# Performance work log

Measured on AMD Instinct MI355X. Metric: run time of the kernel, lower is better.

The kernel has to match this reference:

```python
import jax, jax.numpy as jnp
import numpy as np

EPS_STAB = 1e-9   # numerical_stabilizer default
BN_EPS = 1e-5     # flax BatchNorm default epsilon


def setup_inputs() -> dict:
    key = jax.random.key(0)
    ks = jax.random.split(key, 5)
    B, N, C = 2, 4096, 512
    s = 1.0 / np.sqrt(C)
    d = {"inputs": jax.random.normal(ks[0], (B, N, C), jnp.float32)}
    # 1x1 convs == pointwise linear maps [C_in, C_out] + bias
    for i, w in enumerate(["Wq", "Wk", "Wv", "Wo"]):
        d[w] = jax.random.normal(ks[1 + i], (C, C), jnp.float32) * s
    for b in ["bq", "bk", "bv", "bo"]:
        d[b] = jnp.zeros((C,), jnp.float32)
    # BatchNorm (inference: use_running_average=True since train=False)
    d["bn_scale"] = jnp.ones((C,), jnp.float32)
    d["bn_bias"] = jnp.zeros((C,), jnp.float32)
    d["bn_mean"] = jnp.zeros((C,), jnp.float32)
    d["bn_var"] = jnp.ones((C,), jnp.float32)
    return d


def reference(inputs, Wq, bq, Wk, bk, Wv, bv, Wo, bo,
              bn_scale, bn_bias, bn_mean, bn_var):
    # QKV via 1x1 conv == dense projection. [B, N, C]
    q = inputs @ Wq + bq
    k = inputs @ Wk + bk
    v = inputs @ Wv + bv
    # scores [B, M, N]; softmax over last axis (N)
    att = jax.nn.softmax(jnp.einsum('bmc,bnc->bmn', q, k), axis=-1)
    # non-standard renorm: divide by column sums (axis=1 == M axis)
    att = att / (EPS_STAB + jnp.sum(att, axis=1, keepdims=True))
    # faithful to einsum '...MN,...NC->...NC': sum attention over M, scale v
    out = v * jnp.sum(att, axis=1)[..., None]
    # output 1x1 conv
    out = out @ Wo + bo
    # BatchNorm with running stats (feature axis -1)
    out = (out - bn_mean) * jax.lax.rsqrt(bn_var + BN_EPS) * bn_scale + bn_bias
    return jax.nn.relu(out) + inputs
```

## Files before the change

kernel.cpp:

```cpp
#include <hip/hip_runtime.h>
#include <hip/hip_bf16.h>

typedef unsigned short u16;
typedef __attribute__((ext_vector_type(8))) short short8;
typedef __attribute__((ext_vector_type(4))) float f32x4;

__device__ __forceinline__ u16 f2bf(float f) {
    union { float f; unsigned u; } v; v.f = f;
    unsigned r = v.u + 0x7fffu + ((v.u >> 16) & 1u);
    return (u16)(r >> 16);
}

__device__ __forceinline__ float fexp2(float x) {
#if __has_builtin(__builtin_amdgcn_exp2f)
    return __builtin_amdgcn_exp2f(x);
#else
    return __expf(x * 0.6931471805599453f);
#endif
}

__device__ __forceinline__ void async_cp16(const u16* g, u16* l) {
    __builtin_amdgcn_global_load_lds(
        (const __attribute__((address_space(1))) void*)g,
        (__attribute__((address_space(3))) void*)l, 16, 0, 0);
}

__device__ __forceinline__ void gemm512(const u16* __restrict__ A,
                                        const u16* __restrict__ B,
                                        u16* As, u16* Bs,
                                        f32x4 acc[4][4], int tid) {
    const int lane = tid & 63, w = tid >> 6;
    const int quad = lane >> 4, l15 = lane & 15;
    const int wm = tid >> 7, wn = (tid >> 6) & 1;
    const int srow0 = w * 32 + (lane >> 2);
    const int srow1 = srow0 + 16;
    const int scol = (lane & 3) * 8;
    u16* la0 = As + (w * 2 + 0) * 512;
    u16* la1 = As + (w * 2 + 1) * 512;
    u16* lb0 = Bs + (w * 2 + 0) * 512;
    u16* lb1 = Bs + (w * 2 + 1) * 512;
    for (int k0 = 0; k0 < 512; k0 += 32) {
        __syncthreads();
        async_cp16(A + (size_t)srow0 * 512 + k0 + scol, la0);
        async_cp16(A + (size_t)srow1 * 512 + k0 + scol, la1);
        async_cp16(B + (size_t)srow0 * 512 + k0 + scol, lb0);
        async_cp16(B + (size_t)srow1 * 512 + k0 + scol, lb1);
        __syncthreads();
        short8 af[4], bfr[4];
#pragma unroll
        for (int i = 0; i < 4; i++)
            af[i] = *(const short8*)&As[(wm * 64 + i * 16 + l15) * 32 + quad * 8];
#pragma unroll
        for (int j = 0; j < 4; j++)
            bfr[j] = *(const short8*)&Bs[(wn * 64 + j * 16 + l15) * 32 + quad * 8];
#pragma unroll
        for (int i = 0; i < 4; i++)
#pragma unroll
            for (int j = 0; j < 4; j++)
                acc[i][j] = __builtin_amdgcn_mfma_f32_16x16x32_bf16(
                    af[i], bfr[j], acc[i][j], 0, 0, 0);
    }
}

__global__ void convert_x(const float* __restrict__ X, u16* __restrict__ Xb) {
    int idx = (blockIdx.x * 256 + threadIdx.x) * 4;
    float4 v = *(const float4*)&X[idx];
    ushort4 o;
    o.x = f2bf(v.x); o.y = f2bf(v.y); o.z = f2bf(v.z); o.w = f2bf(v.w);
    *(ushort4*)&Xb[idx] = o;
}

__global__ void transpose_w(const float* __restrict__ W0, const float* __restrict__ W1,
                            const float* __restrict__ W2, const float* __restrict__ W3,
                            u16* __restrict__ T0, u16* __restrict__ T1,
                            u16* __restrict__ T2, u16* __restrict__ T3) {
    const float* src; u16* dst;
    switch (blockIdx.z) {
        case 0: src = W0; dst = T0; break;
        case 1: src = W1; dst = T1; break;
        case 2: src = W2; dst = T2; break;
        default: src = W3; dst = T3; break;
    }
    __shared__ float tile[32][33];
    int bo_ = blockIdx.x * 32;
    int bi  = blockIdx.y * 32;
#pragma unroll
    for (int t = 0; t < 4; t++) {
        int i = bi + threadIdx.y + t * 8;
        tile[threadIdx.y + t * 8][threadIdx.x] = src[i * 512 + bo_ + threadIdx.x];
    }
    __syncthreads();
#pragma unroll
    for (int t = 0; t < 4; t++) {
        int o = bo_ + threadIdx.y + t * 8;
        dst[o * 512 + bi + threadIdx.x] = f2bf(tile[threadIdx.x][threadIdx.y + t * 8]);
    }
}

__global__ __launch_bounds__(256) void gemm_qkv(
    const u16* __restrict__ Xb, const u16* __restrict__ Wall,
    const float* __restrict__ bq, const float* __restrict__ bk,
    const float* __restrict__ bv, u16* __restrict__ Qall) {
    __shared__ __align__(16) u16 As[128 * 32];
    __shared__ __align__(16) u16 Bs[128 * 32];
    int tid = threadIdx.x;
    int m0 = blockIdx.x * 128, n0 = blockIdx.y * 128, z = blockIdx.z;
    const u16* Bt = Wall + (size_t)z * 262144 + (size_t)n0 * 512;
    const float* bias = (z == 0) ? bq : (z == 1) ? bk : bv;
    const float qs = (z == 0) ? 1.44269504088896340736f : 1.0f;
    u16* C = Qall + (size_t)z * 4194304;
    f32x4 acc[4][4];
#pragma unroll
    for (int i = 0; i < 4; i++)
#pragma unroll
        for (int j = 0; j < 4; j++) acc[i][j] = (f32x4){0.f, 0.f, 0.f, 0.f};
    gemm512(Xb + (size_t)m0 * 512, Bt, As, Bs, acc, tid);
    int lane = tid & 63, quad = lane >> 4, l15 = lane & 15;
    int wm = tid >> 7, wn = (tid >> 6) & 1;
#pragma unroll
    for (int j = 0; j < 4; j++) {
        int n = n0 + wn * 64 + j * 16 + l15;
        float bvv = bias[n];
#pragma unroll
        for (int i = 0; i < 4; i++)
#pragma unroll
            for (int rg = 0; rg < 4; rg++) {
                int m = m0 + wm * 64 + i * 16 + quad * 4 + rg;
                C[(size_t)m * 512 + n] = f2bf((acc[i][j][rg] + bvv) * qs);
            }
    }
}

__global__ __launch_bounds__(256) void attn_pass1(
    const u16* __restrict__ Qb, const u16* __restrict__ Kb,
    float2* __restrict__ statsP) {
    __shared__ __align__(16) u16 As[128 * 32];
    __shared__ __align__(16) u16 Bs[128 * 32];
    int tid = threadIdx.x;
    int mblk = blockIdx.x, nch = blockIdx.y, b = blockIdx.z;
    const u16* Q = Qb + ((size_t)(b * 4096 + mblk * 128)) * 512;
    int lane = tid & 63, quad = lane >> 4, l15 = lane & 15;
    int wm = tid >> 7, wn = (tid >> 6) & 1;
    float runM[4][4], runL[4][4];
#pragma unroll
    for (int i = 0; i < 4; i++)
#pragma unroll
        for (int rg = 0; rg < 4; rg++) { runM[i][rg] = -INFINITY; runL[i][rg] = 0.f; }
    for (int nt = 0; nt < 4; nt++) {
        const u16* K = Kb + ((size_t)(b * 4096 + nch * 512 + nt * 128)) * 512;
        f32x4 acc[4][4];
#pragma unroll
        for (int i = 0; i < 4; i++)
#pragma unroll
            for (int j = 0; j < 4; j++) acc[i][j] = (f32x4){0.f, 0.f, 0.f, 0.f};
        gemm512(Q, K, As, Bs, acc, tid);
#pragma unroll
        for (int i = 0; i < 4; i++)
#pragma unroll
            for (int rg = 0; rg < 4; rg++) {
                float v0 = acc[i][0][rg], v1 = acc[i][1][rg];
                float v2 = acc[i][2][rg], v3 = acc[i][3][rg];
                float vm = fmaxf(fmaxf(v0, v1), fmaxf(v2, v3));
                float mo = runM[i][rg];
                if (vm > mo - 30.f) {
                    float nm = fmaxf(mo, vm);
                    runL[i][rg] = runL[i][rg] * fexp2(mo - nm) +
                                  fexp2(v0 - nm) + fexp2(v1 - nm) +
                                  fexp2(v2 - nm) + fexp2(v3 - nm);
                    runM[i][rg] = nm;
                }
            }
    }
#pragma unroll
    for (int i = 0; i < 4; i++)
#pragma unroll
        for (int rg = 0; rg < 4; rg++) {
            float M = runM[i][rg], L = runL[i][rg];
#pragma unroll
            for (int d = 1; d < 16; d <<= 1) {
                float Mo = __shfl_xor(M, d);
                float Lo = __shfl_xor(L, d);
                float Mn = fmaxf(M, Mo);
                L = L * fexp2(M - Mn) + Lo * fexp2(Mo - Mn);
                M = Mn;
            }
            if (l15 == 0)
                statsP[((size_t)(b * 16 + nch * 2 + wn)) * 4096 +
                       mblk * 128 + wm * 64 + i * 16 + quad * 4 + rg] =
                    make_float2(M, L);
        }
}

__global__ void reduce_stats(const float2* __restrict__ statsP,
                             float* __restrict__ cstat) {
    int t = blockIdx.x * 256 + threadIdx.x;
    int b = t >> 12, m = t & 4095;
    float2 p[16];
    float M = -INFINITY;
#pragma unroll
    for (int ch = 0; ch < 16; ch++) {
        p[ch] = statsP[((size_t)(b * 16 + ch)) * 4096 + m];
        M = fmaxf(M, p[ch].x);
    }
    float L = 0.f;
#pragma unroll
    for (int ch = 0; ch < 16; ch++) L += p[ch].y * fexp2(p[ch].x - M);
    cstat[t] = M + __log2f(L);
}

__global__ __launch_bounds__(256) void attn_pass2(
    const u16* __restrict__ Qb, const u16* __restrict__ Kb,
    const float* __restrict__ cstat, float* __restrict__ Sg) {
    __shared__ __align__(16) u16 As[128 * 32];
    __shared__ __align__(16) u16 Bs[128 * 32];
    int tid = threadIdx.x;
    int nblk = blockIdx.x, mch = blockIdx.y, b = blockIdx.z;
    const u16* K = Kb + ((size_t)(b * 4096 + nblk * 128)) * 512;
    int lane = tid & 63, quad = lane >> 4, l15 = lane & 15;
    int wm = tid >> 7, wn = (tid >> 6) & 1;
    float cp0 = 0.f, cp1 = 0.f, cp2 = 0.f, cp3 = 0.f;
    for (int mt = 0; mt < 4; mt++) {
        int m0 = mch * 512 + mt * 128;
        const u16* Q = Qb + ((size_t)(b * 4096 + m0)) * 512;
        f32x4 acc[4][4];
#pragma unroll
        for (int i = 0; i < 4; i++)
#pragma unroll
            for (int j = 0; j < 4; j++) acc[i][j] = (f32x4){0.f, 0.f, 0.f, 0.f};
        gemm512(Q, K, As, Bs, acc, tid);
        float4 c4[4];
#pragma unroll
        for (int i = 0; i < 4; i++)
            c4[i] = *(const float4*)&cstat[b * 4096 + m0 + wm * 64 + i * 16 + quad * 4];
#pragma unroll
        for (int i = 0; i < 4; i++) {
            float cc[4] = {c4[i].x, c4[i].y, c4[i].z, c4[i].w};
#pragma unroll
            for (int rg = 0; rg < 4; rg++) {
                float c = cc[rg];
                float v0 = acc[i][0][rg] - c, v1 = acc[i][1][rg] - c;
                float v2 = acc[i][2][rg] - c, v3 = acc[i][3][rg] - c;
                float vm = fmaxf(fmaxf(v0, v1), fmaxf(v2, v3));
                if (vm > -60.f) {
                    cp0 += fexp2(v0); cp1 += fexp2(v1);
                    cp2 += fexp2(v2); cp3 += fexp2(v3);
                }
            }
        }
    }
    float cps[4] = {cp0, cp1, cp2, cp3};
#pragma unroll
    for (int j = 0; j < 4; j++) {
        float s = cps[j];
        s += __shfl_xor(s, 16);
        s += __shfl_xor(s, 32);
        if (lane < 16)
            atomicAdd(&Sg[b * 4096 + nblk * 128 + wn * 64 + j * 16 + lane], s);
    }
}

__global__ __launch_bounds__(256) void gemm_final(
    const u16* __restrict__ A, const u16* __restrict__ Bt,
    const float* __restrict__ Sg, const float* __restrict__ bo,
    const float* __restrict__ g, const float* __restrict__ bb,
    const float* __restrict__ mean, const float* __restrict__ var,
    const float* __restrict__ X, float* __restrict__ out) {
    __shared__ __align__(16) u16 As[128 * 32];
    __shared__ __align__(16) u16 Bs[128 * 32];
    int tid = threadIdx.x;
    int m0 = blockIdx.x * 128, n0 = blockIdx.y * 128;
    f32x4 acc[4][4];
#pragma unroll
    for (int i = 0; i < 4; i++)
#pragma unroll
        for (int j = 0; j < 4; j++) acc[i][j] = (f32x4){0.f, 0.f, 0.f, 0.f};
    gemm512(A + (size_t)m0 * 512, Bt + (size_t)n0 * 512, As, Bs, acc, tid);
    int lane = tid & 63, quad = lane >> 4, l15 = lane & 15;
    int wm = tid >> 7, wn = (tid >> 6) & 1;
    float sc[4][4];
#pragma unroll
    for (int i = 0; i < 4; i++) {
        float4 s = *(const float4*)&Sg[m0 + wm * 64 + i * 16 + quad * 4];
        float v[4] = {s.x, s.y, s.z, s.w};
#pragma unroll
        for (int rg = 0; rg < 4; rg++) sc[i][rg] = v[rg] / (1e-9f + v[rg]);
    }
#pragma unroll
    for (int j = 0; j < 4; j++) {
        int n = n0 + wn * 64 + j * 16 + l15;
        float aj = rsqrtf(var[n] + 1e-5f) * g[n];
        float cj = bb[n] - mean[n] * aj;
        float bj = bo[n];
#pragma unroll
        for (int i = 0; i < 4; i++)
#pragma unroll
            for (int rg = 0; rg < 4; rg++) {
                int m = m0 + wm * 64 + i * 16 + quad * 4 + rg;
                float x = acc[i][j][rg] * sc[i][rg] + bj;
                float y = x * aj + cj;
                out[(size_t)m * 512 + n] = fmaxf(y, 0.f) + X[(size_t)m * 512 + n];
            }
    }
}

extern "C" void kernel_launch(void* const* d_in, const int* in_sizes, int n_in,
                              void* d_out, int out_size, void* d_ws, size_t ws_size,
                              hipStream_t stream) {
    const float* X  = (const float*)d_in[0];
    const float* Wq = (const float*)d_in[1];
    const float* Wk = (const float*)d_in[2];
    const float* Wv = (const float*)d_in[3];
    const float* Wo = (const float*)d_in[4];
    const float* bq = (const float*)d_in[5];
    const float* bk = (const float*)d_in[6];
    const float* bv = (const float*)d_in[7];
    const float* bo = (const float*)d_in[8];
    const float* g    = (const float*)d_in[9];
    const float* bb   = (const float*)d_in[10];
    const float* mean = (const float*)d_in[11];
    const float* var  = (const float*)d_in[12];
    float* out = (float*)d_out;

    char* ws = (char*)d_ws;
    u16* Xb  = (u16*)(ws + 0);
    u16* Wqt = (u16*)(ws + 8388608);
    u16* Wkt = (u16*)(ws + 8912896);
    u16* Wvt = (u16*)(ws + 9437184);
    u16* Wot = (u16*)(ws + 9961472);
    u16* Qb  = (u16*)(ws + 10485760);
    u16* Kb  = (u16*)(ws + 18874368);
    u16* Vb  = (u16*)(ws + 27262976);
    float2* statsP = (float2*)(ws + 35651584);
    float* cstat   = (float*)(ws + 36700160);
    float* Sg      = (float*)(ws + 36765696);

    convert_x<<<4096, 256, 0, stream>>>(X, Xb);
    transpose_w<<<dim3(16, 16, 4), dim3(32, 8), 0, stream>>>(
        Wq, Wk, Wv, Wo, Wqt, Wkt, Wvt, Wot);
    gemm_qkv<<<dim3(64, 4, 3), 256, 0, stream>>>(Xb, Wqt, bq, bk, bv, Qb);
    attn_pass1<<<dim3(32, 8, 2), 256, 0, stream>>>(Qb, Kb, statsP);
    reduce_stats<<<32, 256, 0, stream>>>(statsP, cstat);
    hipMemsetAsync(Sg, 0, 2 * 4096 * sizeof(float), stream);
    attn_pass2<<<dim3(32, 8, 2), 256, 0, stream>>>(Qb, Kb, cstat, Sg);
    gemm_final<<<dim3(64, 4), 256, 0, stream>>>(Vb, Wot, Sg, bo, g, bb, mean, var,
                                                X, out);
}
```

Before: 235.0 us.

## Double attention grid split, merge prep kernels, fold memset, shrink final GEMM tile

The two attention passes now split the key/query range into 16 chunks of 256 instead of 8 of 512, doubling the grid from 512 to 1024 blocks to fill more compute units. The stats partials grow to 32 per row. The pass-1 shuffle merge is simplified to a max-reduce followed by a sum-reduce. The X conversion and weight transpose are merged into one prep launch, and the Sg zeroing moves into reduce_stats, removing a launch and a memset. The final GEMM uses 64-row tiles to double its block count. The cost is more partial-stat traffic and more redundant Q/K tile loads per block.

```diff
diff --git a/kernel.cpp b/kernel.cpp
--- a/kernel.cpp
+++ b/kernel.cpp
@@ -62,38 +62,78 @@
     }
 }
 
-__global__ void convert_x(const float* __restrict__ X, u16* __restrict__ Xb) {
-    int idx = (blockIdx.x * 256 + threadIdx.x) * 4;
-    float4 v = *(const float4*)&X[idx];
-    ushort4 o;
-    o.x = f2bf(v.x); o.y = f2bf(v.y); o.z = f2bf(v.z); o.w = f2bf(v.w);
-    *(ushort4*)&Xb[idx] = o;
-}
-
-__global__ void transpose_w(const float* __restrict__ W0, const float* __restrict__ W1,
-                            const float* __restrict__ W2, const float* __restrict__ W3,
-                            u16* __restrict__ T0, u16* __restrict__ T1,
-                            u16* __restrict__ T2, u16* __restrict__ T3) {
+__device__ __forceinline__ void gemm512_r64(const u16* __restrict__ A,
+                                            const u16* __restrict__ B,
+                                            u16* As, u16* Bs,
+                                            f32x4 acc[2][4], int tid) {
+    const int lane = tid & 63, w = tid >> 6;
+    const int quad = lane >> 4, l15 = lane & 15;
+    const int wm = tid >> 7, wn = (tid >> 6) & 1;
+    const int srowA = w * 16 + (lane >> 2);
+    const int srowB0 = (w * 2 + 0) * 16 + (lane >> 2);
+    const int srowB1 = (w * 2 + 1) * 16 + (lane >> 2);
+    const int scol = (lane & 3) * 8;
+    u16* la = As + w * 512;
+    u16* lb0 = Bs + (w * 2 + 0) * 512;
+    u16* lb1 = Bs + (w * 2 + 1) * 512;
+    for (int k0 = 0; k0 < 512; k0 += 32) {
+        __syncthreads();
+        async_cp16(A + (size_t)srowA * 512 + k0 + scol, la);
+        async_cp16(B + (size_t)srowB0 * 512 + k0 + scol, lb0);
+        async_cp16(B + (size_t)srowB1 * 512 + k0 + scol, lb1);
+        __syncthreads();
+        short8 af[2], bfr[4];
+#pragma unroll
+        for (int i = 0; i < 2; i++)
+            af[i] = *(const short8*)&As[(wm * 32 + i * 16 + l15) * 32 + quad * 8];
+#pragma unroll
+        for (int j = 0; j < 4; j++)
+            bfr[j] = *(const short8*)&Bs[(wn * 64 + j * 16 + l15) * 32 + quad * 8];
+#pragma unroll
+        for (int i = 0; i < 2; i++)
+#pragma unroll
+            for (int j = 0; j < 4; j++)
+                acc[i][j] = __builtin_amdgcn_mfma_f32_16x16x32_bf16(
+                    af[i], bfr[j], acc[i][j], 0, 0, 0);
+    }
+}
+
+__global__ void prep(const float* __restrict__ X, const float* __restrict__ W0,
+                     const float* __restrict__ W1, const float* __restrict__ W2,
+                     const float* __restrict__ W3, u16* __restrict__ Xb,
+                     u16* __restrict__ T0, u16* __restrict__ T1,
+                     u16* __restrict__ T2, u16* __restrict__ T3) {
+    __shared__ float tile[32][33];
+    int id = blockIdx.x, tid = threadIdx.x;
+    if (id < 4096) {
+        int idx = (id * 256 + tid) * 4;
+        float4 v = *(const float4*)&X[idx];
+        ushort4 o;
+        o.x = f2bf(v.x); o.y = f2bf(v.y); o.z = f2bf(v.z); o.w = f2bf(v.w);
+        *(ushort4*)&Xb[idx] = o;
+        return;
+    }
+    int t = id - 4096;
+    int z = t >> 8, rem = t & 255;
+    int bo_ = (rem & 15) * 32, bi = (rem >> 4) * 32;
     const float* src; u16* dst;
-    switch (blockIdx.z) {
+    switch (z) {
         case 0: src = W0; dst = T0; break;
         case 1: src = W1; dst = T1; break;
         case 2: src = W2; dst = T2; break;
         default: src = W3; dst = T3; break;
     }
-    __shared__ float tile[32][33];
-    int bo_ = blockIdx.x * 32;
-    int bi  = blockIdx.y * 32;
-#pragma unroll
-    for (int t = 0; t < 4; t++) {
-        int i = bi + threadIdx.y + t * 8;
-        tile[threadIdx.y + t * 8][threadIdx.x] = src[i * 512 + bo_ + threadIdx.x];
+    int tx = tid & 31, ty = tid >> 5;
+#pragma unroll
+    for (int s = 0; s < 4; s++) {
+        int i = bi + ty + s * 8;
+        tile[ty + s * 8][tx] = src[i * 512 + bo_ + tx];
     }
     __syncthreads();
 #pragma unroll
-    for (int t = 0; t < 4; t++) {
-        int o = bo_ + threadIdx.y + t * 8;
-        dst[o * 512 + bi + threadIdx.x] = f2bf(tile[threadIdx.x][threadIdx.y + t * 8]);
+    for (int s = 0; s < 4; s++) {
+        int o = bo_ + ty + s * 8;
+        dst[o * 512 + bi + tx] = f2bf(tile[tx][ty + s * 8]);
     }
 }
 
@@ -146,8 +186,8 @@
     for (int i = 0; i < 4; i++)
 #pragma unroll
         for (int rg = 0; rg < 4; rg++) { runM[i][rg] = -INFINITY; runL[i][rg] = 0.f; }
-    for (int nt = 0; nt < 4; nt++) {
-        const u16* K = Kb + ((size_t)(b * 4096 + nch * 512 + nt * 128)) * 512;
+    for (int nt = 0; nt < 2; nt++) {
+        const u16* K = Kb + ((size_t)(b * 4096 + nch * 256 + nt * 128)) * 512;
         f32x4 acc[4][4];
 #pragma unroll
         for (int i = 0; i < 4; i++)
@@ -175,37 +215,36 @@
     for (int i = 0; i < 4; i++)
 #pragma unroll
         for (int rg = 0; rg < 4; rg++) {
-            float M = runM[i][rg], L = runL[i][rg];
-#pragma unroll
-            for (int d = 1; d < 16; d <<= 1) {
-                float Mo = __shfl_xor(M, d);
-                float Lo = __shfl_xor(L, d);
-                float Mn = fmaxf(M, Mo);
-                L = L * fexp2(M - Mn) + Lo * fexp2(Mo - Mn);
-                M = Mn;
-            }
+            float M = runM[i][rg];
+            float Mf = M;
+#pragma unroll
+            for (int d = 1; d < 16; d <<= 1) Mf = fmaxf(Mf, __shfl_xor(Mf, d));
+            float L = runL[i][rg] * fexp2(M - Mf);
+#pragma unroll
+            for (int d = 1; d < 16; d <<= 1) L += __shfl_xor(L, d);
             if (l15 == 0)
-                statsP[((size_t)(b * 16 + nch * 2 + wn)) * 4096 +
+                statsP[((size_t)(b * 32 + nch * 2 + wn)) * 4096 +
                        mblk * 128 + wm * 64 + i * 16 + quad * 4 + rg] =
-                    make_float2(M, L);
+                    make_float2(Mf, L);
         }
 }
 
 __global__ void reduce_stats(const float2* __restrict__ statsP,
-                             float* __restrict__ cstat) {
+                             float* __restrict__ cstat, float* __restrict__ Sg) {
     int t = blockIdx.x * 256 + threadIdx.x;
     int b = t >> 12, m = t & 4095;
-    float2 p[16];
     float M = -INFINITY;
-#pragma unroll
-    for (int ch = 0; ch < 16; ch++) {
-        p[ch] = statsP[((size_t)(b * 16 + ch)) * 4096 + m];
+    float2 p[32];
+#pragma unroll
+    for (int ch = 0; ch < 32; ch++) {
+        p[ch] = statsP[((size_t)(b * 32 + ch)) * 4096 + m];
         M = fmaxf(M, p[ch].x);
     }
     float L = 0.f;
 #pragma unroll
-    for (int ch = 0; ch < 16; ch++) L += p[ch].y * fexp2(p[ch].x - M);
+    for (int ch = 0; ch < 32; ch++) L += p[ch].y * fexp2(p[ch].x - M);
     cstat[t] = M + __log2f(L);
+    Sg[t] = 0.f;
 }
 
 __global__ __launch_bounds__(256) void attn_pass2(
@@ -219,8 +258,8 @@
     int lane = tid & 63, quad = lane >> 4, l15 = lane & 15;
     int wm = tid >> 7, wn = (tid >> 6) & 1;
     float cp0 = 0.f, cp1 = 0.f, cp2 = 0.f, cp3 = 0.f;
-    for (int mt = 0; mt < 4; mt++) {
-        int m0 = mch * 512 + mt * 128;
+    for (int mt = 0; mt < 2; mt++) {
+        int m0 = mch * 256 + mt * 128;
         const u16* Q = Qb + ((size_t)(b * 4096 + m0)) * 512;
         f32x4 acc[4][4];
 #pragma unroll
@@ -265,22 +304,22 @@
     const float* __restrict__ g, const float* __restrict__ bb,
     const float* __restrict__ mean, const float* __restrict__ var,
     const float* __restrict__ X, float* __restrict__ out) {
-    __shared__ __align__(16) u16 As[128 * 32];
+    __shared__ __align__(16) u16 As[64 * 32];
     __shared__ __align__(16) u16 Bs[128 * 32];
     int tid = threadIdx.x;
-    int m0 = blockIdx.x * 128, n0 = blockIdx.y * 128;
-    f32x4 acc[4][4];
-#pragma unroll
-    for (int i = 0; i < 4; i++)
+    int m0 = blockIdx.x * 64, n0 = blockIdx.y * 128;
+    f32x4 acc[2][4];
+#pragma unroll
+    for (int i = 0; i < 2; i++)
 #pragma unroll
         for (int j = 0; j < 4; j++) acc[i][j] = (f32x4){0.f, 0.f, 0.f, 0.f};
-    gemm512(A + (size_t)m0 * 512, Bt + (size_t)n0 * 512, As, Bs, acc, tid);
+    gemm512_r64(A + (size_t)m0 * 512, Bt + (size_t)n0 * 512, As, Bs, acc, tid);
     int lane = tid & 63, quad = lane >> 4, l15 = lane & 15;
     int wm = tid >> 7, wn = (tid >> 6) & 1;
-    float sc[4][4];
-#pragma unroll
-    for (int i = 0; i < 4; i++) {
-        float4 s = *(const float4*)&Sg[m0 + wm * 64 + i * 16 + quad * 4];
+    float sc[2][4];
+#pragma unroll
+    for (int i = 0; i < 2; i++) {
+        float4 s = *(const float4*)&Sg[m0 + wm * 32 + i * 16 + quad * 4];
         float v[4] = {s.x, s.y, s.z, s.w};
 #pragma unroll
         for (int rg = 0; rg < 4; rg++) sc[i][rg] = v[rg] / (1e-9f + v[rg]);
@@ -292,10 +331,10 @@
         float cj = bb[n] - mean[n] * aj;
         float bj = bo[n];
 #pragma unroll
-        for (int i = 0; i < 4; i++)
+        for (int i = 0; i < 2; i++)
 #pragma unroll
             for (int rg = 0; rg < 4; rg++) {
-                int m = m0 + wm * 64 + i * 16 + quad * 4 + rg;
+                int m = m0 + wm * 32 + i * 16 + quad * 4 + rg;
                 float x = acc[i][j][rg] * sc[i][rg] + bj;
                 float y = x * aj + cj;
                 out[(size_t)m * 512 + n] = fmaxf(y, 0.f) + X[(size_t)m * 512 + n];
@@ -331,17 +370,14 @@
     u16* Kb  = (u16*)(ws + 18874368);
     u16* Vb  = (u16*)(ws + 27262976);
     float2* statsP = (float2*)(ws + 35651584);
-    float* cstat   = (float*)(ws + 36700160);
-    float* Sg      = (float*)(ws + 36765696);
-
-    convert_x<<<4096, 256, 0, stream>>>(X, Xb);
-    transpose_w<<<dim3(16, 16, 4), dim3(32, 8), 0, stream>>>(
-        Wq, Wk, Wv, Wo, Wqt, Wkt, Wvt, Wot);
+    float* cstat   = (float*)(ws + 37748736);
+    float* Sg      = (float*)(ws + 37781504);
+
+    prep<<<5120, 256, 0, stream>>>(X, Wq, Wk, Wv, Wo, Xb, Wqt, Wkt, Wvt, Wot);
     gemm_qkv<<<dim3(64, 4, 3), 256, 0, stream>>>(Xb, Wqt, bq, bk, bv, Qb);
-    attn_pass1<<<dim3(32, 8, 2), 256, 0, stream>>>(Qb, Kb, statsP);
-    reduce_stats<<<32, 256, 0, stream>>>(statsP, cstat);
-    hipMemsetAsync(Sg, 0, 2 * 4096 * sizeof(float), stream);
-    attn_pass2<<<dim3(32, 8, 2), 256, 0, stream>>>(Qb, Kb, cstat, Sg);
-    gemm_final<<<dim3(64, 4), 256, 0, stream>>>(Vb, Wot, Sg, bo, g, bb, mean, var,
-                                                X, out);
-}
+    attn_pass1<<<dim3(32, 16, 2), 256, 0, stream>>>(Qb, Kb, statsP);
+    reduce_stats<<<32, 256, 0, stream>>>(statsP, cstat, Sg);
+    attn_pass2<<<dim3(32, 16, 2), 256, 0, stream>>>(Qb, Kb, cstat, Sg);
+    gemm_final<<<dim3(128, 4), 256, 0, stream>>>(Vb, Wot, Sg, bo, g, bb, mean, var,
+                                                 X, out);
+}
```

Result: no change. 234.8 us (-0.1%).
